# Performance work log

Measured on AMD Instinct MI355X. Metric: run time of the kernel, lower is better.

The kernel has to match this reference:

```python
import jax, jax.numpy as jnp
import numpy as np
from jax import lax

C = 64
B, H, W = 4, 192, 192


def conv2d(x, w, b):
    # x: [B,C,H,W], w: [O,I,3,3] (OIHW), stride 1, pad 1
    y = lax.conv_general_dilated(x, w, (1, 1), ((1, 1), (1, 1)),
                                 dimension_numbers=("NCHW", "OIHW", "NCHW"))
    return y + b[None, :, None, None]


def csm(x, w1, b1, w2, b2):
    # residual block: conv3x3 -> relu -> conv3x3 + skip
    return x + conv2d(jax.nn.relu(conv2d(x, w1, b1)), w2, b2)


def setup_inputs() -> dict:
    key = jax.random.key(0)
    ks = jax.random.split(key, 12)
    s = 1.0 / np.sqrt(C * 9)
    def cw(k):
        return jax.random.uniform(k, (C, C, 3, 3), jnp.float32, -s, s)
    def cb(k):
        return jax.random.uniform(k, (C,), jnp.float32, -s, s)
    return {
        "low1": jax.random.normal(ks[0], (B, C, H, W), jnp.float32),
        "low2": jax.random.normal(ks[1], (B, C, H, W), jnp.float32),
        "fe1_w1": cw(ks[2]), "fe1_b1": cb(ks[3]),
        "fe1_w2": cw(ks[4]), "fe1_b2": cb(ks[5]),
        "fe2_w1": cw(ks[6]), "fe2_b1": cb(ks[7]),
        "fe2_w2": cw(ks[8]), "fe2_b2": cb(ks[9]),
        "conv_w": cw(ks[10]), "conv_b": cb(ks[11]),
    }


def reference(low1, low2, fe1_w1, fe1_b1, fe1_w2, fe1_b2,
              fe2_w1, fe2_b1, fe2_w2, fe2_b2, conv_w, conv_b):
    Q1 = conv2d(csm(low1, fe1_w1, fe1_b1, fe1_w2, fe1_b2), conv_w, conv_b)
    K1 = conv2d(csm(low2, fe1_w1, fe1_b1, fe1_w2, fe1_b2), conv_w, conv_b)
    Q2 = conv2d(csm(low1, fe2_w1, fe2_b1, fe2_w2, fe2_b2), conv_w, conv_b)
    K2 = conv2d(csm(low2, fe2_w1, fe2_b1, fe2_w2, fe2_b2), conv_w, conv_b)

    # per-row cross-width scores: [B,H,W,W] (no scaling; softmax then relu)
    score1 = jax.nn.relu(jax.nn.softmax(jnp.einsum("bchw,bchv->bhwv", Q1, K1), axis=-1))
    score2 = jax.nn.relu(jax.nn.softmax(jnp.einsum("bchw,bchv->bhwv", Q2, K2), axis=-1))

    def apply_score(score, feat):
        # out[b,c,h,w] = sum_v score[b,h,w,v] * feat[b,c,h,v]
        return jnp.einsum("bhwv,bchv->bchw", score, feat)

    def apply_score_T(score, feat):
        # out[b,c,h,w] = sum_v score[b,h,v,w] * feat[b,c,h,v]
        return jnp.einsum("bhvw,bchv->bchw", score, feat)

    right2left1 = apply_score(score1, low2)
    right2left2 = apply_score(score2, low2)
    left2right1 = apply_score_T(score1, low1)
    left2right2 = apply_score_T(score2, low1)
    left2right2left = apply_score(score2, left2right1)
    right2left2right = apply_score_T(score2, right2left1)

    left = low1 + right2left1 + right2left2 + left2right2left
    right = low2 + left2right1 + left2right2 + right2left2right
    return (left, right)
```

## Files before the change

### kernel.cpp

```cpp
#include <hip/hip_runtime.h>
#include <stdint.h>

#define NB 4
#define NC 64
#define NH 192
#define NW 192

typedef __attribute__((ext_vector_type(8))) short bf16x8;
typedef __attribute__((ext_vector_type(4))) float f32x4;
typedef unsigned short u16;
typedef unsigned int u32;

__device__ inline float bf2f(u16 x){ u32 u = ((u32)x) << 16; return __builtin_bit_cast(float, u); }
__device__ inline u16 f2bf(float f){ u32 u = __builtin_bit_cast(u32, f); u32 r = u + 0x7fffu + ((u >> 16) & 1u); return (u16)(r >> 16); }
__device__ inline bf16x8 packf8(float4 a, float4 b){
  bf16x8 r;
  r[0]=(short)f2bf(a.x); r[1]=(short)f2bf(a.y); r[2]=(short)f2bf(a.z); r[3]=(short)f2bf(a.w);
  r[4]=(short)f2bf(b.x); r[5]=(short)f2bf(b.y); r[6]=(short)f2bf(b.z); r[7]=(short)f2bf(b.w);
  return r;
}

__global__ void wxform_k(const float* __restrict__ w0, const float* __restrict__ w1,
                         const float* __restrict__ w2, const float* __restrict__ w3,
                         const float* __restrict__ w4, u16* __restrict__ out){
  int idx = blockIdx.x * 256 + threadIdx.x;
  if (idx >= 5 * 36864) return;
  int t = idx / 36864, e = idx % 36864;
  int r = e >> 12, rem = e & 4095, co = rem >> 6, ci = rem & 63;
  const float* src = (t == 0) ? w0 : (t == 1) ? w1 : (t == 2) ? w2 : (t == 3) ? w3 : w4;
  out[idx] = f2bf(src[co * 576 + ci * 9 + r]);
}

__global__ __launch_bounds__(192) void nchw2nhwc_k(const float* __restrict__ in, u16* __restrict__ out){
  int bh = blockIdx.x; int b = bh / NH, h = bh % NH;
  int w = threadIdx.x;
  u16 v[64];
  const float* p = in + ((size_t)b * NC * NH + h) * NW + w;
#pragma unroll
  for (int c = 0; c < 64; ++c) v[c] = f2bf(p[(size_t)c * NH * NW]);
  uint4* q4 = (uint4*)(out + ((size_t)bh * NW + w) * NC);
#pragma unroll
  for (int i = 0; i < 8; ++i){
    uint4 t;
    t.x = (u32)v[i*8+0] | ((u32)v[i*8+1] << 16);
    t.y = (u32)v[i*8+2] | ((u32)v[i*8+3] << 16);
    t.z = (u32)v[i*8+4] | ((u32)v[i*8+5] << 16);
    t.w = (u32)v[i*8+6] | ((u32)v[i*8+7] << 16);
    q4[i] = t;
  }
}

__global__ __launch_bounds__(256) void bf2f_k(const u16* __restrict__ in, float* __restrict__ out){
  int i = blockIdx.x * 256 + threadIdx.x;
  uint4 v = ((const uint4*)in)[i];
  float4 f0, f1;
  f0.x = bf2f((u16)(v.x & 0xffff)); f0.y = bf2f((u16)(v.x >> 16));
  f0.z = bf2f((u16)(v.y & 0xffff)); f0.w = bf2f((u16)(v.y >> 16));
  f1.x = bf2f((u16)(v.z & 0xffff)); f1.y = bf2f((u16)(v.z >> 16));
  f1.z = bf2f((u16)(v.w & 0xffff)); f1.w = bf2f((u16)(v.w >> 16));
  ((float4*)out)[2*i]   = f0;
  ((float4*)out)[2*i+1] = f1;
}

__global__ __launch_bounds__(256) void conv3_k(const u16* __restrict__ in, const u16* __restrict__ wt,
    const float* __restrict__ bias, const u16* __restrict__ skip, u16* __restrict__ out, int relu){
  __shared__ __align__(16) u16 xr[3][98 * 72];
  int blk = blockIdx.x;
  int wh = blk & 1;
  int strip = blk >> 1;
  int g0 = strip * 3;
  int b = g0 / NH, h0 = g0 % NH;
  int wstart = wh * 96;
  int tid = threadIdx.x;
  int wvv = tid >> 6, lane = tid & 63, l15 = lane & 15, qd = lane >> 4;
  int mh = wvv >> 1, wq = wvv & 1;

#define STAGE(hh_) do { \
    int hh = (hh_); \
    int slot = ((hh % 3) + 3) % 3; \
    bool rowok = (hh >= 0) && (hh < NH); \
    const u16* src = in + (((size_t)b * NH + (rowok ? hh : 0)) * NW) * 64; \
    for (int k2 = tid; k2 < 784; k2 += 256){ \
      int x = k2 >> 3, part = k2 & 7; \
      int w = wstart - 1 + x; \
      uint4 val = make_uint4(0,0,0,0); \
      if (rowok && w >= 0 && w < NW) val = *(const uint4*)(src + (size_t)w * 64 + part * 8); \
      *(uint4*)&xr[slot][x * 72 + part * 8] = val; \
    } \
  } while(0)

  STAGE(h0 - 1);
  STAGE(h0);
  for (int j = 0; j < 3; ++j){
    int h = h0 + j;
    STAGE(h + 1);
    __syncthreads();
    f32x4 acc[2][3];
#pragma unroll
    for (int mt = 0; mt < 2; ++mt)
#pragma unroll
      for (int nt = 0; nt < 3; ++nt) acc[mt][nt] = (f32x4){0.f,0.f,0.f,0.f};
#pragma unroll
    for (int r = 0; r < 9; ++r){
      int ky = r / 3, kx = r % 3;
      int hs = h - 1 + ky;
      const u16* xbase = xr[((hs % 3) + 3) % 3];
#pragma unroll
      for (int ks = 0; ks < 2; ++ks){
        int ci = ks * 32 + qd * 8;
        const u16* wp = wt + r * 4096 + ci;
        bf16x8 a0 = *(const bf16x8*)(wp + (mh * 32 + l15) * 64);
        bf16x8 a1 = *(const bf16x8*)(wp + (mh * 32 + 16 + l15) * 64);
#pragma unroll
        for (int nt = 0; nt < 3; ++nt){
          int x = wq * 48 + nt * 16 + l15 + kx;
          bf16x8 bfr = *(const bf16x8*)&xr[0][0 + ((hs % 3) + 3) % 3 * 0];
          bfr = *(const bf16x8*)&xbase[x * 72 + ci];
          acc[0][nt] = __builtin_amdgcn_mfma_f32_16x16x32_bf16(a0, bfr, acc[0][nt], 0, 0, 0);
          acc[1][nt] = __builtin_amdgcn_mfma_f32_16x16x32_bf16(a1, bfr, acc[1][nt], 0, 0, 0);
        }
      }
    }
    size_t rowbase = ((size_t)(b * NH + h)) * NW * 64;
#pragma unroll
    for (int mt = 0; mt < 2; ++mt){
      int co0 = mh * 32 + mt * 16 + qd * 4;
      float4 bb = *(const float4*)(bias + co0);
#pragma unroll
      for (int nt = 0; nt < 3; ++nt){
        int w = wstart + wq * 48 + nt * 16 + l15;
        size_t o = rowbase + (size_t)w * 64 + co0;
        float v0 = acc[mt][nt][0] + bb.x, v1 = acc[mt][nt][1] + bb.y;
        float v2 = acc[mt][nt][2] + bb.z, v3 = acc[mt][nt][3] + bb.w;
        if (relu){ v0 = fmaxf(v0,0.f); v1 = fmaxf(v1,0.f); v2 = fmaxf(v2,0.f); v3 = fmaxf(v3,0.f); }
        if (skip){
          uint2 ss = *(const uint2*)(skip + o);
          v0 += bf2f((u16)(ss.x & 0xffff)); v1 += bf2f((u16)(ss.x >> 16));
          v2 += bf2f((u16)(ss.y & 0xffff)); v3 += bf2f((u16)(ss.y >> 16));
        }
        uint2 st;
        st.x = (u32)f2bf(v0) | ((u32)f2bf(v1) << 16);
        st.y = (u32)f2bf(v2) | ((u32)f2bf(v3) << 16);
        *(uint2*)(out + o) = st;
      }
    }
    __syncthreads();
  }
#undef STAGE
}

template<int XYF32>
__global__ __launch_bounds__(256) void attn_k(const u16* __restrict__ Q, const u16* __restrict__ K,
    const void* __restrict__ Xv, const void* __restrict__ Yv,
    u16* __restrict__ outA, u16* __restrict__ outB){
  __shared__ __align__(16) u16 P [192 * 200];
  __shared__ __align__(16) u16 Pt[192 * 200];
  int bh = blockIdx.x, b = bh / NH, h = bh % NH;
  int tid = threadIdx.x, wv = tid >> 6, lane = tid & 63, l15 = lane & 15, qd = lane >> 4;
  size_t rowo = (size_t)bh * NW * 64;
  const u16* Qr = Q + rowo; const u16* Kr = K + rowo;
  const size_t CS = (size_t)NH * NW;
  size_t xb0 = (size_t)b * 64 * CS + (size_t)h * NW;
  const float* Xf = (const float*)Xv; const float* Yf = (const float*)Yv;
  const u16* Xb = (const u16*)Xv; const u16* Yb = (const u16*)Yv;

#pragma unroll 1
  for (int mi = 0; mi < 3; ++mi){
    int mt = wv * 3 + mi;
    f32x4 s[12];
#pragma unroll
    for (int nt = 0; nt < 12; ++nt) s[nt] = (f32x4){0,0,0,0};
#pragma unroll
    for (int ks = 0; ks < 2; ++ks){
      bf16x8 aq = *(const bf16x8*)(Qr + (mt * 16 + l15) * 64 + ks * 32 + qd * 8);
#pragma unroll
      for (int nt = 0; nt < 12; ++nt){
        bf16x8 bk = *(const bf16x8*)(Kr + (nt * 16 + l15) * 64 + ks * 32 + qd * 8);
        s[nt] = __builtin_amdgcn_mfma_f32_16x16x32_bf16(aq, bk, s[nt], 0, 0, 0);
      }
    }
#pragma unroll
    for (int rg = 0; rg < 4; ++rg){
      float mx = -1e30f;
#pragma unroll
      for (int nt = 0; nt < 12; ++nt) mx = fmaxf(mx, s[nt][rg]);
      mx = fmaxf(mx, __shfl_xor(mx, 1));
      mx = fmaxf(mx, __shfl_xor(mx, 2));
      mx = fmaxf(mx, __shfl_xor(mx, 4));
      mx = fmaxf(mx, __shfl_xor(mx, 8));
      float sum = 0.f;
#pragma unroll
      for (int nt = 0; nt < 12; ++nt){ float ev = __expf(s[nt][rg] - mx); s[nt][rg] = ev; sum += ev; }
      sum += __shfl_xor(sum, 1);
      sum += __shfl_xor(sum, 2);
      sum += __shfl_xor(sum, 4);
      sum += __shfl_xor(sum, 8);
      float inv = 1.f / sum;
      int w = mt * 16 + qd * 4 + rg;
#pragma unroll
      for (int nt = 0; nt < 12; ++nt){
        float val = s[nt][rg] * inv;
        s[nt][rg] = val;
        P[w * 200 + nt * 16 + l15] = f2bf(val);
      }
    }
#pragma unroll
    for (int nt = 0; nt < 12; ++nt){
      uint2 pk;
      pk.x = (u32)f2bf(s[nt][0]) | ((u32)f2bf(s[nt][1]) << 16);
      pk.y = (u32)f2bf(s[nt][2]) | ((u32)f2bf(s[nt][3]) << 16);
      *(uint2*)&Pt[(nt * 16 + l15) * 200 + mt * 16 + qd * 4] = pk;
    }
  }
  __syncthreads();

  f32x4 accA[3][4], accB[3][4];
#pragma unroll
  for (int ni = 0; ni < 3; ++ni)
#pragma unroll
    for (int mt = 0; mt < 4; ++mt){ accA[ni][mt] = (f32x4){0,0,0,0}; accB[ni][mt] = (f32x4){0,0,0,0}; }
#pragma unroll 1
  for (int ks = 0; ks < 6; ++ks){
    int v0 = ks * 32 + qd * 8;
    bf16x8 aX[4], aY[4];
#pragma unroll
    for (int mt = 0; mt < 4; ++mt){
      int c = mt * 16 + l15;
      size_t off = xb0 + (size_t)c * CS + v0;
      if (XYF32){
        float4 x0 = *(const float4*)(Xf + off), x1 = *(const float4*)(Xf + off + 4);
        float4 y0 = *(const float4*)(Yf + off), y1 = *(const float4*)(Yf + off + 4);
        aX[mt] = packf8(x0, x1); aY[mt] = packf8(y0, y1);
      } else {
        aX[mt] = *(const bf16x8*)(Xb + off);
        aY[mt] = *(const bf16x8*)(Yb + off);
      }
    }
#pragma unroll
    for (int ni = 0; ni < 3; ++ni){
      int wrow = (wv * 3 + ni) * 16 + l15;
      bf16x8 bP  = *(const bf16x8*)&P [wrow * 200 + v0];
      bf16x8 bPt = *(const bf16x8*)&Pt[wrow * 200 + v0];
#pragma unroll
      for (int mt = 0; mt < 4; ++mt){
        accA[ni][mt] = __builtin_amdgcn_mfma_f32_16x16x32_bf16(aX[mt], bP,  accA[ni][mt], 0, 0, 0);
        accB[ni][mt] = __builtin_amdgcn_mfma_f32_16x16x32_bf16(aY[mt], bPt, accB[ni][mt], 0, 0, 0);
      }
    }
  }
#pragma unroll
  for (int ni = 0; ni < 3; ++ni){
    int w = (wv * 3 + ni) * 16 + l15;
#pragma unroll
    for (int mt = 0; mt < 4; ++mt){
#pragma unroll
      for (int rg = 0; rg < 4; ++rg){
        int c = mt * 16 + qd * 4 + rg;
        size_t o = xb0 + (size_t)c * CS + w;
        float ra = XYF32 ? Yf[o] : bf2f(Yb[o]);
        float rb = XYF32 ? Xf[o] : bf2f(Xb[o]);
        outA[o] = f2bf(accA[ni][mt][rg] + ra);
        outB[o] = f2bf(accB[ni][mt][rg] + rb);
      }
    }
  }
}

extern "C" void kernel_launch(void* const* d_in, const int* in_sizes, int n_in,
                              void* d_out, int out_size, void* d_ws, size_t ws_size,
                              hipStream_t stream){
  const float* low1 = (const float*)d_in[0];
  const float* low2 = (const float*)d_in[1];
  const float* b11 = (const float*)d_in[3];
  const float* b12 = (const float*)d_in[5];
  const float* b21 = (const float*)d_in[7];
  const float* b22 = (const float*)d_in[9];
  const float* bcv = (const float*)d_in[11];
  const size_t BUF = (size_t)NB * NH * NW * NC;
  u16* WT = (u16*)d_ws;
  u16* s1 = WT + 184320;
  u16* s2 = s1 + BUF;
  u16* o1 = (u16*)d_out;
  u16* o2 = o1 + BUF;
  u16* o3 = o1 + 2 * BUF;
  u16* o4 = o1 + 3 * BUF;
  float* outL = (float*)d_out;
  float* outR = outL + BUF;

  wxform_k<<<dim3(720), dim3(256), 0, stream>>>(
      (const float*)d_in[2], (const float*)d_in[4], (const float*)d_in[6],
      (const float*)d_in[8], (const float*)d_in[10], WT);
  nchw2nhwc_k<<<dim3(NB * NH), dim3(192), 0, stream>>>(low1, o1);
  nchw2nhwc_k<<<dim3(NB * NH), dim3(192), 0, stream>>>(low2, o2);

#define CONV(in_, wti, bias_, skip_, out_, relu_) \
  conv3_k<<<dim3(512), dim3(256), 0, stream>>>(in_, WT + (wti) * 36864, bias_, skip_, out_, relu_)

  CONV(o1, 0, b11, (const u16*)nullptr, o3, 1);
  CONV(o3, 1, b12, o1, o4, 0);
  CONV(o4, 4, bcv, (const u16*)nullptr, s1, 0);
  CONV(o2, 0, b11, (const u16*)nullptr, o3, 1);
  CONV(o3, 1, b12, o2, o4, 0);
  CONV(o4, 4, bcv, (const u16*)nullptr, s2, 0);
  attn_k<1><<<dim3(NB * NH), dim3(256), 0, stream>>>(s1, s2, (const void*)low2, (const void*)low1, o3, o4);
  CONV(o1, 2, b21, (const u16*)nullptr, s1, 1);
  CONV(s1, 3, b22, o1, s2, 0);
  CONV(s2, 4, bcv, (const u16*)nullptr, o1, 0);
  CONV(o2, 2, b21, (const u16*)nullptr, s1, 1);
  CONV(s1, 3, b22, o2, s2, 0);
  CONV(s2, 4, bcv, (const u16*)nullptr, o2, 0);
  attn_k<0><<<dim3(NB * NH), dim3(256), 0, stream>>>(o1, o2, (const void*)o4, (const void*)o3, s1, s2);
  bf2f_k<<<dim3((int)(BUF / 8 / 256)), dim3(256), 0, stream>>>(s1, outL);
  bf2f_k<<<dim3((int)(BUF / 8 / 256)), dim3(256), 0, stream>>>(s2, outR);
#undef CONV
}
```

Measured before the change: 638.6 us.

## Split conv rows into thirds and share one P buffer via in-place transpose

The conv kernel now splits each row strip into three 64-wide pieces instead of two 96-wide halves. That shrinks shared memory, gives 768 blocks instead of 512, and uses fewer accumulators, at the cost of more halo reloads. The attention kernel drops the separate Pt buffer, halving its LDS use so more blocks can be resident per CU. It computes the P·X product, transposes P in place in shared memory, then computes the Pᵀ·Y product. This adds an extra sync, a scalar 16-bit LDS transpose pass, and serialises the two GEMMs that were previously interleaved.

```diff
diff --git a/kernel.cpp b/kernel.cpp
--- a/kernel.cpp
+++ b/kernel.cpp
@@ -64,13 +64,13 @@
 
 __global__ __launch_bounds__(256) void conv3_k(const u16* __restrict__ in, const u16* __restrict__ wt,
     const float* __restrict__ bias, const u16* __restrict__ skip, u16* __restrict__ out, int relu){
-  __shared__ __align__(16) u16 xr[3][98 * 72];
+  __shared__ __align__(16) u16 xr[3][66 * 72];
   int blk = blockIdx.x;
-  int wh = blk & 1;
-  int strip = blk >> 1;
+  int wp = blk % 3;
+  int strip = blk / 3;
   int g0 = strip * 3;
   int b = g0 / NH, h0 = g0 % NH;
-  int wstart = wh * 96;
+  int wstart = wp * 64;
   int tid = threadIdx.x;
   int wvv = tid >> 6, lane = tid & 63, l15 = lane & 15, qd = lane >> 4;
   int mh = wvv >> 1, wq = wvv & 1;
@@ -80,7 +80,7 @@
     int slot = ((hh % 3) + 3) % 3; \
     bool rowok = (hh >= 0) && (hh < NH); \
     const u16* src = in + (((size_t)b * NH + (rowok ? hh : 0)) * NW) * 64; \
-    for (int k2 = tid; k2 < 784; k2 += 256){ \
+    for (int k2 = tid; k2 < 528; k2 += 256){ \
       int x = k2 >> 3, part = k2 & 7; \
       int w = wstart - 1 + x; \
       uint4 val = make_uint4(0,0,0,0); \
@@ -95,11 +95,11 @@
     int h = h0 + j;
     STAGE(h + 1);
     __syncthreads();
-    f32x4 acc[2][3];
+    f32x4 acc[2][2];
 #pragma unroll
     for (int mt = 0; mt < 2; ++mt)
 #pragma unroll
-      for (int nt = 0; nt < 3; ++nt) acc[mt][nt] = (f32x4){0.f,0.f,0.f,0.f};
+      for (int nt = 0; nt < 2; ++nt) acc[mt][nt] = (f32x4){0.f,0.f,0.f,0.f};
 #pragma unroll
     for (int r = 0; r < 9; ++r){
       int ky = r / 3, kx = r % 3;
@@ -108,14 +108,13 @@
 #pragma unroll
       for (int ks = 0; ks < 2; ++ks){
         int ci = ks * 32 + qd * 8;
-        const u16* wp = wt + r * 4096 + ci;
-        bf16x8 a0 = *(const bf16x8*)(wp + (mh * 32 + l15) * 64);
-        bf16x8 a1 = *(const bf16x8*)(wp + (mh * 32 + 16 + l15) * 64);
-#pragma unroll
-        for (int nt = 0; nt < 3; ++nt){
-          int x = wq * 48 + nt * 16 + l15 + kx;
-          bf16x8 bfr = *(const bf16x8*)&xr[0][0 + ((hs % 3) + 3) % 3 * 0];
-          bfr = *(const bf16x8*)&xbase[x * 72 + ci];
+        const u16* wp_ = wt + r * 4096 + ci;
+        bf16x8 a0 = *(const bf16x8*)(wp_ + (mh * 32 + l15) * 64);
+        bf16x8 a1 = *(const bf16x8*)(wp_ + (mh * 32 + 16 + l15) * 64);
+#pragma unroll
+        for (int nt = 0; nt < 2; ++nt){
+          int x = wq * 32 + nt * 16 + l15 + kx;
+          bf16x8 bfr = *(const bf16x8*)&xbase[x * 72 + ci];
           acc[0][nt] = __builtin_amdgcn_mfma_f32_16x16x32_bf16(a0, bfr, acc[0][nt], 0, 0, 0);
           acc[1][nt] = __builtin_amdgcn_mfma_f32_16x16x32_bf16(a1, bfr, acc[1][nt], 0, 0, 0);
         }
@@ -127,8 +126,8 @@
       int co0 = mh * 32 + mt * 16 + qd * 4;
       float4 bb = *(const float4*)(bias + co0);
 #pragma unroll
-      for (int nt = 0; nt < 3; ++nt){
-        int w = wstart + wq * 48 + nt * 16 + l15;
+      for (int nt = 0; nt < 2; ++nt){
+        int w = wstart + wq * 32 + nt * 16 + l15;
         size_t o = rowbase + (size_t)w * 64 + co0;
         float v0 = acc[mt][nt][0] + bb.x, v1 = acc[mt][nt][1] + bb.y;
         float v2 = acc[mt][nt][2] + bb.z, v3 = acc[mt][nt][3] + bb.w;
@@ -153,8 +152,7 @@
 __global__ __launch_bounds__(256) void attn_k(const u16* __restrict__ Q, const u16* __restrict__ K,
     const void* __restrict__ Xv, const void* __restrict__ Yv,
     u16* __restrict__ outA, u16* __restrict__ outB){
-  __shared__ __align__(16) u16 P [192 * 200];
-  __shared__ __align__(16) u16 Pt[192 * 200];
+  __shared__ __align__(16) u16 P[192 * 200];
   int bh = blockIdx.x, b = bh / NH, h = bh % NH;
   int tid = threadIdx.x, wv = tid >> 6, lane = tid & 63, l15 = lane & 15, qd = lane >> 4;
   size_t rowo = (size_t)bh * NW * 64;
@@ -199,68 +197,135 @@
       int w = mt * 16 + qd * 4 + rg;
 #pragma unroll
       for (int nt = 0; nt < 12; ++nt){
-        float val = s[nt][rg] * inv;
-        s[nt][rg] = val;
-        P[w * 200 + nt * 16 + l15] = f2bf(val);
-      }
-    }
-#pragma unroll
-    for (int nt = 0; nt < 12; ++nt){
-      uint2 pk;
-      pk.x = (u32)f2bf(s[nt][0]) | ((u32)f2bf(s[nt][1]) << 16);
-      pk.y = (u32)f2bf(s[nt][2]) | ((u32)f2bf(s[nt][3]) << 16);
-      *(uint2*)&Pt[(nt * 16 + l15) * 200 + mt * 16 + qd * 4] = pk;
-    }
-  }
+        P[w * 200 + nt * 16 + l15] = f2bf(s[nt][rg] * inv);
+      }
+    }
+  }
+
+  {
+    f32x4 accA[3][4];
+#pragma unroll
+    for (int ni = 0; ni < 3; ++ni)
+#pragma unroll
+      for (int mt = 0; mt < 4; ++mt) accA[ni][mt] = (f32x4){0,0,0,0};
+#pragma unroll 1
+    for (int ks = 0; ks < 6; ++ks){
+      int v0 = ks * 32 + qd * 8;
+      bf16x8 aX[4];
+#pragma unroll
+      for (int mt = 0; mt < 4; ++mt){
+        int c = mt * 16 + l15;
+        size_t off = xb0 + (size_t)c * CS + v0;
+        if (XYF32){
+          float4 x0 = *(const float4*)(Xf + off), x1 = *(const float4*)(Xf + off + 4);
+          aX[mt] = packf8(x0, x1);
+        } else {
+          aX[mt] = *(const bf16x8*)(Xb + off);
+        }
+      }
+#pragma unroll
+      for (int ni = 0; ni < 3; ++ni){
+        int wrow = (wv * 3 + ni) * 16 + l15;
+        bf16x8 bP = *(const bf16x8*)&P[wrow * 200 + v0];
+#pragma unroll
+        for (int mt = 0; mt < 4; ++mt){
+          accA[ni][mt] = __builtin_amdgcn_mfma_f32_16x16x32_bf16(aX[mt], bP, accA[ni][mt], 0, 0, 0);
+        }
+      }
+    }
+#pragma unroll
+    for (int ni = 0; ni < 3; ++ni){
+      int w = (wv * 3 + ni) * 16 + l15;
+#pragma unroll
+      for (int mt = 0; mt < 4; ++mt){
+#pragma unroll
+        for (int rg = 0; rg < 4; ++rg){
+          int c = mt * 16 + qd * 4 + rg;
+          size_t o = xb0 + (size_t)c * CS + w;
+          float ra = XYF32 ? Yf[o] : bf2f(Yb[o]);
+          outA[o] = f2bf(accA[ni][mt][rg] + ra);
+        }
+      }
+    }
+  }
+
   __syncthreads();
 
-  f32x4 accA[3][4], accB[3][4];
-#pragma unroll
-  for (int ni = 0; ni < 3; ++ni)
-#pragma unroll
-    for (int mt = 0; mt < 4; ++mt){ accA[ni][mt] = (f32x4){0,0,0,0}; accB[ni][mt] = (f32x4){0,0,0,0}; }
+  {
+    int r = tid >> 4, c = tid & 15;
 #pragma unroll 1
-  for (int ks = 0; ks < 6; ++ks){
-    int v0 = ks * 32 + qd * 8;
-    bf16x8 aX[4], aY[4];
-#pragma unroll
-    for (int mt = 0; mt < 4; ++mt){
-      int c = mt * 16 + l15;
-      size_t off = xb0 + (size_t)c * CS + v0;
-      if (XYF32){
-        float4 x0 = *(const float4*)(Xf + off), x1 = *(const float4*)(Xf + off + 4);
-        float4 y0 = *(const float4*)(Yf + off), y1 = *(const float4*)(Yf + off + 4);
-        aX[mt] = packf8(x0, x1); aY[mt] = packf8(y0, y1);
-      } else {
-        aX[mt] = *(const bf16x8*)(Xb + off);
-        aY[mt] = *(const bf16x8*)(Yb + off);
+    for (int TI = 0; TI < 12; ++TI){
+      if (c > r){
+        u16 a = P[(TI*16 + r)*200 + TI*16 + c];
+        u16 d = P[(TI*16 + c)*200 + TI*16 + r];
+        P[(TI*16 + r)*200 + TI*16 + c] = d;
+        P[(TI*16 + c)*200 + TI*16 + r] = a;
+      }
+      int TJ = TI + 1;
+      for (; TJ + 1 < 12; TJ += 2){
+        u16 a0 = P[(TI*16 + r)*200 + TJ*16 + c];
+        u16 b0 = P[(TJ*16 + c)*200 + TI*16 + r];
+        u16 a1 = P[(TI*16 + r)*200 + (TJ+1)*16 + c];
+        u16 b1 = P[((TJ+1)*16 + c)*200 + TI*16 + r];
+        P[(TI*16 + r)*200 + TJ*16 + c] = b0;
+        P[(TJ*16 + c)*200 + TI*16 + r] = a0;
+        P[(TI*16 + r)*200 + (TJ+1)*16 + c] = b1;
+        P[((TJ+1)*16 + c)*200 + TI*16 + r] = a1;
+      }
+      if (TJ < 12){
+        u16 a0 = P[(TI*16 + r)*200 + TJ*16 + c];
+        u16 b0 = P[(TJ*16 + c)*200 + TI*16 + r];
+        P[(TI*16 + r)*200 + TJ*16 + c] = b0;
+        P[(TJ*16 + c)*200 + TI*16 + r] = a0;
+      }
+    }
+  }
+
+  __syncthreads();
+
+  {
+    f32x4 accB[3][4];
+#pragma unroll
+    for (int ni = 0; ni < 3; ++ni)
+#pragma unroll
+      for (int mt = 0; mt < 4; ++mt) accB[ni][mt] = (f32x4){0,0,0,0};
+#pragma unroll 1
+    for (int ks = 0; ks < 6; ++ks){
+      int v0 = ks * 32 + qd * 8;
+      bf16x8 aY[4];
+#pragma unroll
+      for (int mt = 0; mt < 4; ++mt){
+        int c = mt * 16 + l15;
+        size_t off = xb0 + (size_t)c * CS + v0;
+        if (XYF32){
+          float4 y0 = *(const float4*)(Yf + off), y1 = *(const float4*)(Yf + off + 4);
+          aY[mt] = packf8(y0, y1);
+        } else {
+          aY[mt] = *(const bf16x8*)(Yb + off);
+        }
+      }
+#pragma unroll
+      for (int ni = 0; ni < 3; ++ni){
+        int wrow = (wv * 3 + ni) * 16 + l15;
+        bf16x8 bPt = *(const bf16x8*)&P[wrow * 200 + v0];
+#pragma unroll
+        for (int mt = 0; mt < 4; ++mt){
+          accB[ni][mt] = __builtin_amdgcn_mfma_f32_16x16x32_bf16(aY[mt], bPt, accB[ni][mt], 0, 0, 0);
+        }
       }
     }
 #pragma unroll
     for (int ni = 0; ni < 3; ++ni){
-      int wrow = (wv * 3 + ni) * 16 + l15;
-      bf16x8 bP  = *(const bf16x8*)&P [wrow * 200 + v0];
-      bf16x8 bPt = *(const bf16x8*)&Pt[wrow * 200 + v0];
+      int w = (wv * 3 + ni) * 16 + l15;
 #pragma unroll
       for (int mt = 0; mt < 4; ++mt){
-        accA[ni][mt] = __builtin_amdgcn_mfma_f32_16x16x32_bf16(aX[mt], bP,  accA[ni][mt], 0, 0, 0);
-        accB[ni][mt] = __builtin_amdgcn_mfma_f32_16x16x32_bf16(aY[mt], bPt, accB[ni][mt], 0, 0, 0);
-      }
-    }
-  }
-#pragma unroll
-  for (int ni = 0; ni < 3; ++ni){
-    int w = (wv * 3 + ni) * 16 + l15;
-#pragma unroll
-    for (int mt = 0; mt < 4; ++mt){
-#pragma unroll
-      for (int rg = 0; rg < 4; ++rg){
-        int c = mt * 16 + qd * 4 + rg;
-        size_t o = xb0 + (size_t)c * CS + w;
-        float ra = XYF32 ? Yf[o] : bf2f(Yb[o]);
-        float rb = XYF32 ? Xf[o] : bf2f(Xb[o]);
-        outA[o] = f2bf(accA[ni][mt][rg] + ra);
-        outB[o] = f2bf(accB[ni][mt][rg] + rb);
+#pragma unroll
+        for (int rg = 0; rg < 4; ++rg){
+          int c = mt * 16 + qd * 4 + rg;
+          size_t o = xb0 + (size_t)c * CS + w;
+          float rb = XYF32 ? Xf[o] : bf2f(Xb[o]);
+          outB[o] = f2bf(accB[ni][mt][rg] + rb);
+        }
       }
     }
   }
@@ -294,7 +359,7 @@
   nchw2nhwc_k<<<dim3(NB * NH), dim3(192), 0, stream>>>(low2, o2);
 
 #define CONV(in_, wti, bias_, skip_, out_, relu_) \
-  conv3_k<<<dim3(512), dim3(256), 0, stream>>>(in_, WT + (wti) * 36864, bias_, skip_, out_, relu_)
+  conv3_k<<<dim3(768), dim3(256), 0, stream>>>(in_, WT + (wti) * 36864, bias_, skip_, out_, relu_)
 
   CONV(o1, 0, b11, (const u16*)nullptr, o3, 1);
   CONV(o3, 1, b12, o1, o4, 0);
```

Result: slower. 770.2 us (+20.6%).
